# Optimization experiments

Hardware: AMD Instinct MI355X
Metric: run time of the kernel (lower is better)

The kernel has to match this reference:

```python
import jax, jax.numpy as jnp
import numpy as np

B, S, H = 1, 2048, 2048
NH = 16
HS = H // NH  # 128
NEG = -65504.0  # fp16 min used as additive mask value


def setup_inputs() -> dict:
    key = jax.random.key(0)
    k1, k2, k3, k4, k5 = jax.random.split(key, 5)
    hidden_states = jax.random.normal(k1, (B, S, H), dtype=jnp.float32)
    # causal left-to-right mask: 1 where attention allowed
    ltor_mask = jnp.tril(jnp.ones((S, S), dtype=jnp.float32))[None, None, :, :]
    W_qkv = jax.random.normal(k2, (H, 3 * H), dtype=jnp.float32) * (1.0 / np.sqrt(H))
    b_qkv = jax.random.normal(k3, (3 * H,), dtype=jnp.float32) * 0.01
    W_dense = jax.random.normal(k4, (H, H), dtype=jnp.float32) * (1.0 / np.sqrt(H))
    b_dense = jax.random.normal(k5, (H,), dtype=jnp.float32) * 0.01
    return {"hidden_states": hidden_states, "ltor_mask": ltor_mask,
            "W_qkv": W_qkv, "b_qkv": b_qkv, "W_dense": W_dense, "b_dense": b_dense}


def reference(hidden_states, ltor_mask, W_qkv, b_qkv, W_dense, b_dense):
    b, s, h = hidden_states.shape
    # fused QKV projection, then split along last dim (matches split_tensor_along_last_dim)
    qkv = hidden_states @ W_qkv + b_qkv  # [b, s, 3h]
    q, k, v = jnp.split(qkv, 3, axis=-1)
    q = q.reshape(b, s, NH, HS)
    k = k.reshape(b, s, NH, HS)
    v = v.reshape(b, s, NH, HS)
    scale = 1.0 / np.sqrt(HS)  # softmax_scale=None -> 1/sqrt(headdim)
    scores = jnp.einsum('bqhd,bkhd->bhqk', q, k) * scale
    scores = scores + NEG * (1.0 - ltor_mask)  # additive mask, [b,1,s,s] broadcast over heads
    probs = jax.nn.softmax(scores, axis=-1)
    ctx = jnp.einsum('bhqk,bkhd->bqhd', probs, v).reshape(b, s, h)
    out = ctx @ W_dense + b_dense  # output_dropout is identity in eval
    return out
```

## Files before the change

kernel.cpp:

```cpp
#include <hip/hip_runtime.h>
#include <math.h>

#define S_LEN 2048
#define HDIM  2048
#define NHEAD 16
#define HSZ   128
#define H3    6144

typedef __attribute__((ext_vector_type(8))) short bf16x8;
typedef __attribute__((ext_vector_type(4))) float f32x4;

__device__ inline ushort f2bf(float f) {
    union { float f; unsigned u; } c; c.f = f;
    unsigned u = c.u;
    return (ushort)((u + 0x7fffu + ((u >> 16) & 1u)) >> 16);
}
__device__ inline ushort f2bf_trunc(float f) {
    union { float f; unsigned u; } c; c.f = f;
    return (ushort)(c.u >> 16);
}

__global__ __launch_bounds__(256) void prep(
    const float* __restrict__ X,    ushort* __restrict__ Xb,
    const float* __restrict__ Wqkv, ushort* __restrict__ Wqt,
    const float* __restrict__ Wd,   ushort* __restrict__ Wdt)
{
    __shared__ ushort t[64][66];
    const int bid = blockIdx.x;
    const int tid = threadIdx.x;

    if (bid < 4096) {
        int i = bid * 1024 + tid * 4;
        float4 v = *(const float4*)(X + i);
        ushort4 o;
        o.x = f2bf(v.x); o.y = f2bf(v.y); o.z = f2bf(v.z); o.w = f2bf(v.w);
        *(ushort4*)(Xb + i) = o;
        return;
    }

    const float* W; ushort* Wt; int K, N, n0, k0;
    if (bid < 7168) {
        const int b = bid - 4096;
        W = Wqkv; Wt = Wqt; K = HDIM; N = H3;
        n0 = (b % 96) * 64; k0 = (b / 96) * 64;
    } else {
        const int b = bid - 7168;
        W = Wd; Wt = Wdt; K = HDIM; N = HDIM;
        n0 = (b % 32) * 64; k0 = (b / 32) * 64;
    }
    const int tx = tid & 15;
    const int ty = tid >> 4;
    #pragma unroll
    for (int p = 0; p < 4; p++) {
        const int k = p * 16 + ty;
        float4 v = *(const float4*)(&W[(size_t)(k0 + k) * N + n0 + tx * 4]);
        t[k][tx * 4 + 0] = f2bf(v.x);
        t[k][tx * 4 + 1] = f2bf(v.y);
        t[k][tx * 4 + 2] = f2bf(v.z);
        t[k][tx * 4 + 3] = f2bf(v.w);
    }
    __syncthreads();
    #pragma unroll
    for (int p = 0; p < 4; p++) {
        const int n = p * 16 + ty;
        ushort4 o;
        o.x = t[tx * 4 + 0][n];
        o.y = t[tx * 4 + 1][n];
        o.z = t[tx * 4 + 2][n];
        o.w = t[tx * 4 + 3][n];
        *(ushort4*)(&Wt[(size_t)(n0 + n) * K + k0 + tx * 4]) = o;
    }
}

__global__ __launch_bounds__(256) void transpose_v(const ushort* __restrict__ qkvb,
                                                   ushort* __restrict__ Vtb) {
    __shared__ ushort t[64][66];
    const int s0 = blockIdx.x * 64;
    const int d0 = blockIdx.y * 64;
    const int tx = threadIdx.x & 15;
    const int ty = threadIdx.x >> 4;
    #pragma unroll
    for (int p = 0; p < 4; p++) {
        const int s = p * 16 + ty;
        ushort4 v = *(const ushort4*)(&qkvb[(size_t)(s0 + s) * H3 + 2 * HDIM + d0 + tx * 4]);
        *(ushort4*)(&t[s][tx * 4]) = v;
    }
    __syncthreads();
    #pragma unroll
    for (int p = 0; p < 4; p++) {
        const int d = p * 16 + ty;
        ushort4 o;
        o.x = t[tx * 4 + 0][d];
        o.y = t[tx * 4 + 1][d];
        o.z = t[tx * 4 + 2][d];
        o.w = t[tx * 4 + 3][d];
        *(ushort4*)(&Vtb[(size_t)(d0 + d) * S_LEN + s0 + tx * 4]) = o;
    }
}

__global__ __launch_bounds__(256, 2) void gemm_qkv_v4(
    const ushort* __restrict__ A, const ushort* __restrict__ Bt,
    const float* __restrict__ bias, ushort* __restrict__ Cb,
    int M, int N, int K)
{
    __shared__ __align__(16) ushort lds[2][128 * 64 + 192 * 64];

    const int tid  = threadIdx.x;
    const int m0   = blockIdx.y * 128;
    const int n0   = blockIdx.x * 192;
    const int w    = tid >> 6;
    const int wm   = w >> 1;
    const int wn   = w & 1;
    const int lane = tid & 63;
    const int quad = lane >> 4;
    const int l16  = lane & 15;

    const int rdsw = l16 & 7;

    f32x4 acc[4][6] = {};

    const int T = K / 64;

    auto stage = [&](int kt) {
        const int b  = kt & 1;
        const int k0 = kt * 64;
        #pragma unroll
        for (int r = 0; r < 4; r++) {
            const int c   = r * 256 + tid;
            const int row = c >> 3;
            const int csw = ((c & 7) ^ (row & 7)) * 8;
            const ushort* ga = A + (size_t)(m0 + row) * K + k0 + csw;
            __builtin_amdgcn_global_load_lds(
                (const __attribute__((address_space(1))) void*)ga,
                (__attribute__((address_space(3))) void*)(&lds[b][0] + c * 8), 16, 0, 0);
        }
        #pragma unroll
        for (int r = 0; r < 6; r++) {
            const int c   = r * 256 + tid;
            const int row = c >> 3;
            const int csw = ((c & 7) ^ (row & 7)) * 8;
            const ushort* gb = Bt + (size_t)(n0 + row) * K + k0 + csw;
            __builtin_amdgcn_global_load_lds(
                (const __attribute__((address_space(1))) void*)gb,
                (__attribute__((address_space(3))) void*)(&lds[b][8192] + c * 8), 16, 0, 0);
        }
    };

    stage(0);

    for (int u = 0; u < T; u++) {
        const int b = u & 1;
        if (u + 1 < T) {
            stage(u + 1);
            asm volatile("s_waitcnt vmcnt(10)" ::: "memory");
        } else {
            asm volatile("s_waitcnt vmcnt(0)" ::: "memory");
        }
        asm volatile("s_barrier" ::: "memory");

        const ushort* bA = &lds[b][0];
        const ushort* bB = &lds[b][8192];

        bf16x8 af[4][2], bq[6][2];
        #pragma unroll
        for (int i = 0; i < 4; i++)
            #pragma unroll
            for (int kc = 0; kc < 2; kc++)
                af[i][kc] = *(const bf16x8*)(bA + (wm * 64 + i * 16 + l16) * 64
                                               + ((((kc << 2) | quad) ^ rdsw) * 8));
        #pragma unroll
        for (int j = 0; j < 6; j++)
            #pragma unroll
            for (int kc = 0; kc < 2; kc++)
                bq[j][kc] = *(const bf16x8*)(bB + (wn * 96 + j * 16 + l16) * 64
                                               + ((((kc << 2) | quad) ^ rdsw) * 8));

        __builtin_amdgcn_s_setprio(1);
        #pragma unroll
        for (int i = 0; i < 4; i++)
            #pragma unroll
            for (int j = 0; j < 6; j++)
                #pragma unroll
                for (int kc = 0; kc < 2; kc++)
                    acc[i][j] = __builtin_amdgcn_mfma_f32_16x16x32_bf16(
                        af[i][kc], bq[j][kc], acc[i][j], 0, 0, 0);
        __builtin_amdgcn_s_setprio(0);

        asm volatile("s_waitcnt lgkmcnt(0)" ::: "memory");
        asm volatile("s_barrier" ::: "memory");
    }

    #pragma unroll
    for (int i = 0; i < 4; i++) {
        #pragma unroll
        for (int r = 0; r < 4; r++) {
            const int m = m0 + wm * 64 + i * 16 + quad * 4 + r;
            #pragma unroll
            for (int j = 0; j < 6; j++) {
                const int n = n0 + wn * 96 + j * 16 + l16;
                float v  = acc[i][j][r] + bias[n];
                float vp = __shfl_xor(v, 1, 64);
                unsigned both = (unsigned)f2bf(v) | ((unsigned)f2bf(vp) << 16);
                if ((l16 & 1) == 0)
                    *(unsigned*)(Cb + (size_t)m * N + n) = both;
            }
        }
    }
}

__global__ __launch_bounds__(256) void gemm_dense(
    const ushort* __restrict__ A, const ushort* __restrict__ Bt,
    const float* __restrict__ bias, float* __restrict__ C)
{
    __shared__ ushort sA[2 * 64 * 32];
    __shared__ ushort sB[2 * 128 * 32];

    const int tid  = threadIdx.x;
    const int m0   = blockIdx.y * 64;
    const int n0   = blockIdx.x * 128;
    const int w    = tid >> 6;
    const int lane = tid & 63;
    const int quad = lane >> 4;
    const int l16  = lane & 15;
    const int wr   = (w >> 1) * 32;
    const int wc   = (w & 1) * 64;

    f32x4 acc[2][4] = {};

    for (int k0 = 0; k0 < HDIM; k0 += 64) {
        #pragma unroll
        for (int iss = 0; iss < 2; iss++) {
            const int li  = iss * 256 + tid;
            const int c   = li >> 8;
            const int row = (li >> 2) & 63;
            const int kc  = (li & 3) * 8;
            const ushort* ga = A + (size_t)(m0 + row) * HDIM + k0 + c * 32 + kc;
            __builtin_amdgcn_global_load_lds(
                (const __attribute__((address_space(1))) void*)ga,
                (__attribute__((address_space(3))) void*)(sA + li * 8), 16, 0, 0);
        }
        #pragma unroll
        for (int iss = 0; iss < 4; iss++) {
            const int li  = iss * 256 + tid;
            const int c   = li >> 9;
            const int row = (li >> 2) & 127;
            const int kc  = (li & 3) * 8;
            const ushort* gb = Bt + (size_t)(n0 + row) * HDIM + k0 + c * 32 + kc;
            __builtin_amdgcn_global_load_lds(
                (const __attribute__((address_space(1))) void*)gb,
                (__attribute__((address_space(3))) void*)(sB + li * 8), 16, 0, 0);
        }
        __syncthreads();

        #pragma unroll
        for (int c = 0; c < 2; c++) {
            bf16x8 af[2], bq[4];
            #pragma unroll
            for (int i = 0; i < 2; i++)
                af[i] = *(const bf16x8*)(sA + c * 2048 + (wr + i * 16 + l16) * 32 + quad * 8);
            #pragma unroll
            for (int j = 0; j < 4; j++)
                bq[j] = *(const bf16x8*)(sB + c * 4096 + (wc + j * 16 + l16) * 32 + quad * 8);

            #pragma unroll
            for (int i = 0; i < 2; i++)
                #pragma unroll
                for (int j = 0; j < 4; j++)
                    acc[i][j] = __builtin_amdgcn_mfma_f32_16x16x32_bf16(
                        af[i], bq[j], acc[i][j], 0, 0, 0);
        }
        __syncthreads();
    }

    #pragma unroll
    for (int i = 0; i < 2; i++)
        #pragma unroll
        for (int r = 0; r < 4; r++) {
            const int m = m0 + wr + i * 16 + quad * 4 + r;
            #pragma unroll
            for (int j = 0; j < 4; j++) {
                const int n = n0 + wc + j * 16 + l16;
                C[(size_t)m * HDIM + n] = acc[i][j][r] + bias[n];
            }
        }
}

__global__ __launch_bounds__(256) void attn_mfma(
    const ushort* __restrict__ qkvb, const ushort* __restrict__ Vtb,
    ushort* __restrict__ ctxb)
{
    __shared__ __align__(16) ushort sK [2][64 * 128];
    __shared__ __align__(16) ushort sVt[2][128 * 64];
    __shared__ __align__(16) ushort Ps [4 * 1024];

    const int tid  = threadIdx.x;
    const int bid  = blockIdx.x;
    const int h    = bid & 15;
    const int qt   = (bid < 256) ? (31 - (bid >> 4)) : ((bid - 256) >> 4);
    const int q0   = qt * 64;
    const int w    = tid >> 6;
    const int lane = tid & 63;
    const int quad = lane >> 4;
    const int l16  = lane & 15;
    const int qr0  = q0 + w * 16;

    const float scale = 0.08838834764831845f;

    bf16x8 qf[4];
    #pragma unroll
    for (int c = 0; c < 4; c++)
        qf[c] = *(const bf16x8*)(qkvb + (size_t)(qr0 + l16) * H3 + h * HSZ + c * 32 + quad * 8);

    f32x4 o[8] = {};
    float lsum[4] = {0.f, 0.f, 0.f, 0.f};

    const int nt   = qt + 1;
    const int skey = tid >> 2;
    const int sq8  = tid & 3;

    auto stage = [&](int kt, int b) {
        const int k0 = kt * 64;
        #pragma unroll
        for (int iss = 0; iss < 4; iss++) {
            const int li = iss * 256 + tid;
            const ushort* g = qkvb + (size_t)(k0 + skey) * H3 + HDIM + h * HSZ + iss * 32 + sq8 * 8;
            __builtin_amdgcn_global_load_lds(
                (const __attribute__((address_space(1))) void*)g,
                (__attribute__((address_space(3))) void*)(&sK[b][0] + li * 8), 16, 0, 0);
        }
        #pragma unroll
        for (int iss = 0; iss < 4; iss++) {
            const int li = iss * 256 + tid;
            const int c  = li >> 9;
            const int d  = (li >> 2) & 127;
            const ushort* g = Vtb + (size_t)(h * HSZ + d) * S_LEN + k0 + c * 32 + (li & 3) * 8;
            __builtin_amdgcn_global_load_lds(
                (const __attribute__((address_space(1))) void*)g,
                (__attribute__((address_space(3))) void*)(&sVt[b][0] + li * 8), 16, 0, 0);
        }
    };

    stage(0, 0);
    const int wofs = w * 1024;

    for (int kt = 0; kt < nt; kt++) {
        const int b  = kt & 1;
        const int k0 = kt * 64;

        if (kt + 1 < nt) {
            stage(kt + 1, b ^ 1);
            asm volatile("s_waitcnt vmcnt(8)" ::: "memory");
        } else {
            asm volatile("s_waitcnt vmcnt(0)" ::: "memory");
        }
        asm volatile("s_barrier" ::: "memory");

        const ushort* bK = &sK[b][0];
        const ushort* bV = &sVt[b][0];

        f32x4 sacc[4] = {};
        #pragma unroll
        for (int jt = 0; jt < 4; jt++)
            #pragma unroll
            for (int c = 0; c < 4; c++) {
                bf16x8 kf = *(const bf16x8*)(bK + c * 2048 + (jt * 16 + l16) * 32 + quad * 8);
                sacc[jt] = __builtin_amdgcn_mfma_f32_16x16x32_bf16(qf[c], kf, sacc[jt], 0, 0, 0);
            }

        float p[4][4];
        if (kt == nt - 1) {
            #pragma unroll
            for (int jt = 0; jt < 4; jt++) {
                const int key = k0 + jt * 16 + l16;
                #pragma unroll
                for (int r = 0; r < 4; r++) {
                    float e = __expf(sacc[jt][r] * scale);
                    if (key > qr0 + quad * 4 + r) e = 0.f;
                    p[jt][r] = e;
                    lsum[r] += e;
                }
            }
        } else {
            #pragma unroll
            for (int jt = 0; jt < 4; jt++)
                #pragma unroll
                for (int r = 0; r < 4; r++) {
                    float e = __expf(sacc[jt][r] * scale);
                    p[jt][r] = e;
                    lsum[r] += e;
                }
        }

        #pragma unroll
        for (int jt = 0; jt < 4; jt++) {
            const int cpan = jt >> 1;
            const int lch  = (jt & 1) * 2 + (l16 >> 3);
            const int phys = lch ^ quad;
            #pragma unroll
            for (int r = 0; r < 4; r++) {
                const int row = quad * 4 + r;
                Ps[wofs + cpan * 512 + row * 32 + phys * 8 + (l16 & 7)] = f2bf_trunc(p[jt][r]);
            }
        }

        #pragma unroll
        for (int c = 0; c < 2; c++) {
            const int pph = quad ^ (l16 >> 2);
            bf16x8 pf = *(const bf16x8*)(Ps + wofs + c * 512 + l16 * 32 + pph * 8);
            #pragma unroll
            for (int ht = 0; ht < 8; ht++) {
                bf16x8 vf = *(const bf16x8*)(bV + c * 4096 + (ht * 16 + l16) * 32 + quad * 8);
                o[ht] = __builtin_amdgcn_mfma_f32_16x16x32_bf16(pf, vf, o[ht], 0, 0, 0);
            }
        }

        asm volatile("s_waitcnt lgkmcnt(0)" ::: "memory");
        asm volatile("s_barrier" ::: "memory");
    }

    float invl[4];
    #pragma unroll
    for (int r = 0; r < 4; r++) {
        float ls = lsum[r];
        #pragma unroll
        for (int off = 1; off < 16; off <<= 1)
            ls += __shfl_xor(ls, off, 64);
        invl[r] = 1.0f / ls;
    }
    #pragma unroll
    for (int ht = 0; ht < 8; ht++) {
        #pragma unroll
        for (int r = 0; r < 4; r++) {
            float v  = o[ht][r] * invl[r];
            float vp = __shfl_xor(v, 1, 64);
            unsigned both = (unsigned)f2bf(v) | ((unsigned)f2bf(vp) << 16);
            if ((l16 & 1) == 0)
                *(unsigned*)(ctxb + (size_t)(qr0 + quad * 4 + r) * HDIM + h * HSZ + ht * 16 + l16) = both;
        }
    }
}

extern "C" void kernel_launch(void* const* d_in, const int* in_sizes, int n_in,
                              void* d_out, int out_size, void* d_ws, size_t ws_size,
                              hipStream_t stream) {
    const float* X    = (const float*)d_in[0];
    const float* Wqkv = (const float*)d_in[2];
    const float* bqkv = (const float*)d_in[3];
    const float* Wd   = (const float*)d_in[4];
    const float* bd   = (const float*)d_in[5];
    float* out = (float*)d_out;

    ushort* Xb   = (ushort*)d_ws;
    ushort* Wqt  = Xb   + (size_t)S_LEN * HDIM;
    ushort* Wdt  = Wqt  + (size_t)H3 * HDIM;
    ushort* ctxb = Wdt  + (size_t)HDIM * HDIM;
    ushort* qkvb = ctxb + (size_t)S_LEN * HDIM;
    ushort* Vtb  = qkvb + (size_t)S_LEN * H3;

    dim3 blk(256);

    prep<<<dim3(8192), blk, 0, stream>>>(X, Xb, Wqkv, Wqt, Wd, Wdt);

    gemm_qkv_v4<<<dim3(H3 / 192, S_LEN / 128), blk, 0, stream>>>(
        Xb, Wqt, bqkv, qkvb, S_LEN, H3, HDIM);

    transpose_v<<<dim3(S_LEN / 64, HDIM / 64), blk, 0, stream>>>(qkvb, Vtb);

    attn_mfma<<<dim3(512), blk, 0, stream>>>(qkvb, Vtb, ctxb);

    gemm_dense<<<dim3(HDIM / 128, S_LEN / 64), blk, 0, stream>>>(
        ctxb, Wdt, bd, out);
}
```

Baseline: 275.9 us.

## Split causal attention key range in two with separate combine kernel

```diff
diff --git a/kernel.cpp b/kernel.cpp
--- a/kernel.cpp
+++ b/kernel.cpp
@@ -285,18 +285,25 @@
         }
 }
 
-__global__ __launch_bounds__(256) void attn_mfma(
+__global__ __launch_bounds__(256) void attn_split(
     const ushort* __restrict__ qkvb, const ushort* __restrict__ Vtb,
-    ushort* __restrict__ ctxb)
+    float* __restrict__ po, float* __restrict__ ctxf)
 {
     __shared__ __align__(16) ushort sK [2][64 * 128];
     __shared__ __align__(16) ushort sVt[2][128 * 64];
     __shared__ __align__(16) ushort Ps [4 * 1024];
 
-    const int tid  = threadIdx.x;
-    const int bid  = blockIdx.x;
-    const int h    = bid & 15;
-    const int qt   = (bid < 256) ? (31 - (bid >> 4)) : ((bid - 256) >> 4);
+    const int tid = threadIdx.x;
+    const int bid = blockIdx.x;
+    const int qt  = 31 - (bid >> 5);
+    const int rem = bid & 31;
+    const int h   = rem >> 1;
+    const int sh  = rem & 1;
+    const int nt  = qt + 1;
+    const int h0  = (nt + 1) >> 1;
+    const int ks  = sh ? h0 : 0;
+    const int ke  = sh ? nt : h0;
+
     const int q0   = qt * 64;
     const int w    = tid >> 6;
     const int lane = tid & 63;
@@ -314,7 +321,6 @@
     f32x4 o[8] = {};
     float lsum[4] = {0.f, 0.f, 0.f, 0.f};
 
-    const int nt   = qt + 1;
     const int skey = tid >> 2;
     const int sq8  = tid & 3;
 
@@ -340,14 +346,14 @@
         }
     };
 
-    stage(0, 0);
+    if (ks < ke) stage(ks, 0);
     const int wofs = w * 1024;
 
-    for (int kt = 0; kt < nt; kt++) {
-        const int b  = kt & 1;
+    for (int kt = ks; kt < ke; kt++) {
+        const int b  = (kt - ks) & 1;
         const int k0 = kt * 64;
 
-        if (kt + 1 < nt) {
+        if (kt + 1 < ke) {
             stage(kt + 1, b ^ 1);
             asm volatile("s_waitcnt vmcnt(8)" ::: "memory");
         } else {
@@ -368,7 +374,7 @@
             }
 
         float p[4][4];
-        if (kt == nt - 1) {
+        if (kt == qt) {
             #pragma unroll
             for (int jt = 0; jt < 4; jt++) {
                 const int key = k0 + jt * 16 + l16;
@@ -418,26 +424,66 @@
         asm volatile("s_barrier" ::: "memory");
     }
 
-    float invl[4];
+    float* poS = po + (size_t)sh * S_LEN * HDIM;
+
     #pragma unroll
     for (int r = 0; r < 4; r++) {
         float ls = lsum[r];
         #pragma unroll
         for (int off = 1; off < 16; off <<= 1)
             ls += __shfl_xor(ls, off, 64);
-        invl[r] = 1.0f / ls;
+        const int row = qr0 + quad * 4 + r;
+        if (l16 == 0)
+            ctxf[(size_t)row * 1024 + sh * 16 + h] = ls;
     }
     #pragma unroll
     for (int ht = 0; ht < 8; ht++) {
         #pragma unroll
         for (int r = 0; r < 4; r++) {
-            float v  = o[ht][r] * invl[r];
+            const int row = qr0 + quad * 4 + r;
+            float v  = o[ht][r];
             float vp = __shfl_xor(v, 1, 64);
-            unsigned both = (unsigned)f2bf(v) | ((unsigned)f2bf(vp) << 16);
-            if ((l16 & 1) == 0)
-                *(unsigned*)(ctxb + (size_t)(qr0 + quad * 4 + r) * HDIM + h * HSZ + ht * 16 + l16) = both;
-        }
-    }
+            if ((l16 & 1) == 0) {
+                float2 t; t.x = v; t.y = vp;
+                *(float2*)(poS + (size_t)row * HDIM + h * HSZ + ht * 16 + l16) = t;
+            }
+        }
+    }
+}
+
+__global__ __launch_bounds__(256) void attn_combine(
+    const float* __restrict__ po, const float* __restrict__ ctxf,
+    ushort* __restrict__ ctxb)
+{
+    __shared__ float linv[16];
+    const int row = blockIdx.x;
+    const int tid = threadIdx.x;
+
+    if (tid < 16) {
+        float l0 = ctxf[(size_t)row * 1024 + tid];
+        float l1 = ctxf[(size_t)row * 1024 + 16 + tid];
+        linv[tid] = 1.0f / (l0 + l1);
+    }
+    __syncthreads();
+
+    const float* r0 = po + (size_t)row * HDIM;
+    const float* r1 = po + (size_t)S_LEN * HDIM + (size_t)row * HDIM;
+    const int c0 = tid * 8;
+    const float s = linv[c0 >> 7];
+
+    float4 a0 = *(const float4*)(r0 + c0);
+    float4 b0 = *(const float4*)(r1 + c0);
+    float4 a1 = *(const float4*)(r0 + c0 + 4);
+    float4 b1 = *(const float4*)(r1 + c0 + 4);
+
+    ushort4 u0, u1;
+    u0.x = f2bf((a0.x + b0.x) * s); u0.y = f2bf((a0.y + b0.y) * s);
+    u0.z = f2bf((a0.z + b0.z) * s); u0.w = f2bf((a0.w + b0.w) * s);
+    u1.x = f2bf((a1.x + b1.x) * s); u1.y = f2bf((a1.y + b1.y) * s);
+    u1.z = f2bf((a1.z + b1.z) * s); u1.w = f2bf((a1.w + b1.w) * s);
+
+    *(ushort4*)(ctxb + (size_t)row * HDIM + c0)     = u0;
+    *(ushort4*)(ctxb + (size_t)row * HDIM + c0 + 4) = u1;
 }
 
 extern "C" void kernel_launch(void* const* d_in, const int* in_sizes, int n_in,
@@ -457,6 +503,9 @@
     ushort* qkvb = ctxb + (size_t)S_LEN * HDIM;
     ushort* Vtb  = qkvb + (size_t)S_LEN * H3;
 
+    float* po   = (float*)d_ws;
+    float* ctxf = (float*)ctxb;
+
     dim3 blk(256);
 
     prep<<<dim3(8192), blk, 0, stream>>>(X, Xb, Wqkv, Wqt, Wd, Wdt);
@@ -466,7 +515,9 @@
 
     transpose_v<<<dim3(S_LEN / 64, HDIM / 64), blk, 0, stream>>>(qkvb, Vtb);
 
-    attn_mfma<<<dim3(512), blk, 0, stream>>>(qkvb, Vtb, ctxb);
+    attn_split<<<dim3(1024), blk, 0, stream>>>(qkvb, Vtb, po, ctxf);
+
+    attn_combine<<<dim3(S_LEN), blk, 0, stream>>>(po, ctxf, ctxb);
 
     gemm_dense<<<dim3(HDIM / 128, S_LEN / 64), blk, 0, stream>>>(
         ctxb, Wdt, bd, out);
```

Result: faster. 268.1 us (-2.8%).
